# Kernel optimization log

Measured on AMD Instinct MI355X. Metric: run time of the kernel, lower is better.

## Reference

```python
import jax, jax.numpy as jnp
import numpy as np

D_MODEL = 768
NHEAD = 12
DK = D_MODEL // NHEAD
MAX_DIST = 1000.0
FF = 3072
POS_HIDDEN = 32  # hidden width of the relative-position bias MLP
EPS = 1e-5
B, L = 2, 1024


def setup_inputs() -> dict:
    key = jax.random.key(0)
    ks = jax.random.split(key, 24)

    def lin(k, i, o):  # torch-Linear-like init, stored as (in, out)
        return jax.random.uniform(k, (i, o), jnp.float32, -1.0, 1.0) / np.sqrt(i)

    return {
        "src": jax.random.normal(ks[0], (B, L, D_MODEL), jnp.float32),
        "src_x": jax.random.uniform(ks[1], (B, L), jnp.float32) * 1000.0,
        "src_y": jax.random.uniform(ks[2], (B, L), jnp.float32) * 1000.0,
        # attention projections (q,k,v,out)
        "Wq": lin(ks[3], D_MODEL, D_MODEL), "bq": jnp.zeros((D_MODEL,), jnp.float32),
        "Wk": lin(ks[4], D_MODEL, D_MODEL), "bk": jnp.zeros((D_MODEL,), jnp.float32),
        "Wv": lin(ks[5], D_MODEL, D_MODEL), "bv": jnp.zeros((D_MODEL,), jnp.float32),
        "Wo": lin(ks[6], D_MODEL, D_MODEL), "bo": jnp.zeros((D_MODEL,), jnp.float32),
        # relative-position bias MLP: 2 -> POS_HIDDEN -> NHEAD
        "P1": lin(ks[7], 2, POS_HIDDEN), "pb1": jnp.zeros((POS_HIDDEN,), jnp.float32),
        "P2": lin(ks[8], POS_HIDDEN, NHEAD), "pb2": jnp.zeros((NHEAD,), jnp.float32),
        # FFN
        "W1": lin(ks[9], D_MODEL, FF), "b1": jnp.zeros((FF,), jnp.float32),
        "W2": lin(ks[10], FF, D_MODEL), "b2": jnp.zeros((D_MODEL,), jnp.float32),
        # post-LN params
        "g1": jnp.ones((D_MODEL,), jnp.float32), "be1": jnp.zeros((D_MODEL,), jnp.float32),
        "g2": jnp.ones((D_MODEL,), jnp.float32), "be2": jnp.zeros((D_MODEL,), jnp.float32),
    }


def _layernorm(x, g, b):
    m = jnp.mean(x, axis=-1, keepdims=True)
    v = jnp.var(x, axis=-1, keepdims=True)
    return (x - m) * jax.lax.rsqrt(v + EPS) * g + b


def reference(src, src_x, src_y, Wq, bq, Wk, bk, Wv, bv, Wo, bo,
              P1, pb1, P2, pb2, W1, b1, W2, b2, g1, be1, g2, be2):
    b, l, _ = src.shape
    # projections -> (b, h, l, dk)
    q = (src @ Wq + bq).reshape(b, l, NHEAD, DK).transpose(0, 2, 1, 3)
    k = (src @ Wk + bk).reshape(b, l, NHEAD, DK).transpose(0, 2, 1, 3)
    v = (src @ Wv + bv).reshape(b, l, NHEAD, DK).transpose(0, 2, 1, 3)
    # 2D relative positions, clipped and normalized to [-1, 1]
    rx = jnp.clip(src_x[:, :, None] - src_x[:, None, :], -MAX_DIST, MAX_DIST) / MAX_DIST
    ry = jnp.clip(src_y[:, :, None] - src_y[:, None, :], -MAX_DIST, MAX_DIST) / MAX_DIST
    rel = jnp.stack([rx, ry], axis=-1)                        # (b, l, l, 2)
    bias = jax.nn.relu(rel @ P1 + pb1) @ P2 + pb2             # (b, l, l, h)
    bias = bias.transpose(0, 3, 1, 2)                         # (b, h, l, l)
    scores = jnp.einsum('bhqd,bhkd->bhqk', q, k) / np.sqrt(DK).astype(np.float32) + bias
    attn = jax.nn.softmax(scores, axis=-1)
    o = jnp.einsum('bhqk,bhkd->bhqd', attn, v).transpose(0, 2, 1, 3).reshape(b, l, D_MODEL)
    src2 = o @ Wo + bo
    x = _layernorm(src + src2, g1, be1)                       # post-LN residual 1
    ff = jax.nn.relu(x @ W1 + b1) @ W2 + b2                   # FFN
    return _layernorm(x + ff, g2, be2)                        # post-LN residual 2
```

## Files before the change

### kernel.cpp

```cpp
#include <hip/hip_runtime.h>
#include <math.h>

typedef unsigned short ushort_t;
typedef __attribute__((ext_vector_type(8))) short bf16x8;
typedef __attribute__((ext_vector_type(4))) float f32x4;

constexpr int kD      = 768;
constexpr int kNH     = 12;
constexpr int kDK     = 64;
constexpr int kFF     = 3072;
constexpr int kL      = 1024;
constexpr int kRows   = 2048;
constexpr float kEPS  = 1e-5f;

__device__ __forceinline__ ushort_t f2bf(float f) {
    union { float f; unsigned u; } v; v.f = f;
    unsigned r = (v.u + 0x7fffu + ((v.u >> 16) & 1u)) >> 16;
    return (ushort_t)r;
}
__device__ __forceinline__ float bf2f(ushort_t u) {
    union { unsigned u; float f; } v; v.u = ((unsigned)u) << 16; return v.f;
}

#define GL_LDS(gp, lp) __builtin_amdgcn_global_load_lds( \
    (const __attribute__((address_space(1))) void*)(gp), \
    (__attribute__((address_space(3))) void*)(lp), 16, 0, 0)

template<int RELU, int OUTBF, int ADDBIAS>
__device__ __forceinline__ void gemm_body(const ushort_t* __restrict__ A,
                                          const ushort_t* __restrict__ WT,
                                          const float* __restrict__ bias,
                                          void* __restrict__ Cout,
                                          int N, int K, int row0, int col0,
                                          int kbeg, int kend)
{
    __shared__ ushort_t lds[8192];
    ushort_t* As = lds;
    ushort_t* Bs = lds + 4096;

    const int tid  = threadIdx.x;
    const int lane = tid & 63;
    const int wave = tid >> 6;
    const int wrow = (wave & 1) * 64;
    const int wcol = (wave >> 1) * 64;

    const int srow = wave * 16 + (lane >> 2);
    const int sk   = (lane & 3) * 8;
    const ushort_t* ga0 = A  + (size_t)(row0 + srow)      * K + sk;
    const ushort_t* ga1 = A  + (size_t)(row0 + srow + 64) * K + sk;
    const ushort_t* gb0 = WT + (size_t)(col0 + srow)      * K + sk;
    const ushort_t* gb1 = WT + (size_t)(col0 + srow + 64) * K + sk;
    ushort_t* la0 = As + wave * 512;
    ushort_t* la1 = As + 2048 + wave * 512;
    ushort_t* lb0 = Bs + wave * 512;
    ushort_t* lb1 = Bs + 2048 + wave * 512;

    const int fl = lane & 15, fq = lane >> 4;
    const ushort_t* fa[4];
    const ushort_t* fb[4];
    #pragma unroll
    for (int i = 0; i < 4; ++i) {
        fa[i] = As + (wrow + i * 16 + fl) * 32 + fq * 8;
        fb[i] = Bs + (wcol + i * 16 + fl) * 32 + fq * 8;
    }

    f32x4 acc[4][4] = {};

    for (int k0 = kbeg; k0 < kend; k0 += 32) {
        __syncthreads();
        GL_LDS(ga0 + k0, la0);
        GL_LDS(ga1 + k0, la1);
        GL_LDS(gb0 + k0, lb0);
        GL_LDS(gb1 + k0, lb1);
        __syncthreads();

        bf16x8 av[4], bv[4];
        #pragma unroll
        for (int i = 0; i < 4; ++i) {
            av[i] = *(const bf16x8*)fa[i];
            bv[i] = *(const bf16x8*)fb[i];
        }
        #pragma unroll
        for (int mi = 0; mi < 4; ++mi)
            #pragma unroll
            for (int ni = 0; ni < 4; ++ni)
                acc[mi][ni] = __builtin_amdgcn_mfma_f32_16x16x32_bf16(
                    av[mi], bv[ni], acc[mi][ni], 0, 0, 0);
    }

    #pragma unroll
    for (int mi = 0; mi < 4; ++mi) {
        const int m = wrow + mi * 16 + fq * 4;
        #pragma unroll
        for (int ni = 0; ni < 4; ++ni) {
            const int n = wcol + ni * 16 + fl;
            const float bb = ADDBIAS ? bias[col0 + n] : 0.f;
            #pragma unroll
            for (int r = 0; r < 4; ++r) {
                float v = acc[mi][ni][r] + bb;
                if (RELU) v = fmaxf(v, 0.f);
                const size_t idx = (size_t)(row0 + m + r) * N + col0 + n;
                if (OUTBF) ((ushort_t*)Cout)[idx] = f2bf(v);
                else       ((float*)Cout)[idx]    = v;
            }
        }
    }
}

template<int RELU, int OUTBF>
__global__ __launch_bounds__(256)
void gemm_kernel(const ushort_t* __restrict__ A, const ushort_t* __restrict__ WT,
                 const float* __restrict__ bias, void* __restrict__ Cout,
                 int N, int K)
{
    gemm_body<RELU, OUTBF, 1>(A, WT, bias, Cout, N, K,
                              blockIdx.y * 128, blockIdx.x * 128, 0, K);
}

__global__ __launch_bounds__(256)
void gemm_splitk_kernel(const ushort_t* __restrict__ A, const ushort_t* __restrict__ WT,
                        float* __restrict__ parts, int N, int K, int kslice)
{
    const int z = blockIdx.z;
    float* out = parts + (size_t)z * kRows * N;
    gemm_body<0, 0, 0>(A, WT, nullptr, out, N, K,
                       blockIdx.y * 128, blockIdx.x * 128, z * kslice, (z + 1) * kslice);
}

__global__ __launch_bounds__(256)
void gemm_qkv_kernel(const ushort_t* __restrict__ A,
                     const ushort_t* wq, const ushort_t* wk, const ushort_t* wv,
                     const float* bq, const float* bk, const float* bv,
                     ushort_t* q, ushort_t* k, ushort_t* v)
{
    const ushort_t* WT; const float* bias; ushort_t* out;
    if (blockIdx.z == 0)      { WT = wq; bias = bq; out = q; }
    else if (blockIdx.z == 1) { WT = wk; bias = bk; out = k; }
    else                      { WT = wv; bias = bv; out = v; }
    gemm_body<0, 1, 1>(A, WT, bias, out, kD, kD,
                       blockIdx.y * 128, blockIdx.x * 128, 0, kD);
}

struct WtDesc { const float* src; ushort_t* dst; int K; int N; };
struct WtArgs { WtDesc d[3]; };

__global__ __launch_bounds__(256)
void wt_kernel(WtArgs args)
{
    const WtDesc w = args.d[blockIdx.z];
    const int ktiles = w.K >> 6;
    const int kt = (blockIdx.x % ktiles) * 64;
    const int nt = (blockIdx.x / ktiles) * 64;
    if (nt >= w.N) return;

    __shared__ float T[64][65];
    const int tid = threadIdx.x;
    #pragma unroll
    for (int i = 0; i < 4; ++i) {
        const int e = tid + i * 256;
        const int r = e >> 4;
        const int c = (e & 15) * 4;
        const float4 f = *(const float4*)&w.src[(size_t)(kt + r) * w.N + nt + c];
        T[c + 0][r] = f.x; T[c + 1][r] = f.y; T[c + 2][r] = f.z; T[c + 3][r] = f.w;
    }
    __syncthreads();
    #pragma unroll
    for (int i = 0; i < 4; ++i) {
        const int e = tid + i * 256;
        const int n = e >> 4;
        const int kc = (e & 15) * 4;
        ushort4 o;
        o.x = f2bf(T[n][kc + 0]); o.y = f2bf(T[n][kc + 1]);
        o.z = f2bf(T[n][kc + 2]); o.w = f2bf(T[n][kc + 3]);
        *(ushort4*)&w.dst[(size_t)(nt + n) * w.K + kt + kc] = o;
    }
}

__global__ __launch_bounds__(256)
void cvt_kernel(const float* __restrict__ in, ushort_t* __restrict__ out, int n4)
{
    const int i = blockIdx.x * 256 + threadIdx.x;
    if (i < n4) {
        const float4 f = ((const float4*)in)[i];
        ushort4 o;
        o.x = f2bf(f.x); o.y = f2bf(f.y); o.z = f2bf(f.z); o.w = f2bf(f.w);
        ((ushort4*)out)[i] = o;
    }
}

__global__ __launch_bounds__(256)
void vtrans_kernel(const ushort_t* __restrict__ vb, ushort_t* __restrict__ vt)
{
    const int bh = blockIdx.x;
    const int b = bh / kNH, h = bh - b * kNH;
    const int j0 = blockIdx.y * 64;
    __shared__ ushort_t T[64][72];

    const int tid = threadIdx.x;
    {
        const int jr = tid & 63;
        const int c0 = (tid >> 6) * 16;
        const ushort_t* sp = vb + (size_t)(b * kL + j0 + jr) * kD + h * kDK + c0;
        uint4 u0 = *(const uint4*)sp;
        uint4 u1 = *(const uint4*)(sp + 8);
        const ushort_t* e0 = (const ushort_t*)&u0;
        const ushort_t* e1 = (const ushort_t*)&u1;
        #pragma unroll
        for (int jj = 0; jj < 8; ++jj) {
            T[c0 + jj][jr]     = e0[jj];
            T[c0 + 8 + jj][jr] = e1[jj];
        }
    }
    __syncthreads();
    {
        const int dr = tid >> 2;
        const int jc = (tid & 3) * 16;
        ushort_t* dp = vt + (size_t)(bh * 64 + dr) * kL + j0 + jc;
        *(uint4*)dp       = *(const uint4*)&T[dr][jc];
        *(uint4*)(dp + 8) = *(const uint4*)&T[dr][jc + 8];
    }
}

__global__ __launch_bounds__(256)
void bias_kernel(const float* __restrict__ sx, const float* __restrict__ sy,
                 const float* __restrict__ P1, const float* __restrict__ pb1,
                 const float* __restrict__ P2, const float* __restrict__ pb2,
                 ushort_t* __restrict__ biasb)
{
    const int bid = blockIdx.x;
    const int b = bid >> 12;
    const int i = (bid >> 2) & 1023;
    const int j = (bid & 3) * 256 + threadIdx.x;
    const int tid = threadIdx.x;

    __shared__ float A1[32], B1[32], C1[32], W2l[384], pb2l[12];
    if (tid < 32) { A1[tid] = P1[tid]; B1[tid] = P1[32 + tid]; C1[tid] = pb1[tid]; }
    if (tid < 12) pb2l[tid] = pb2[tid];
    for (int e = tid; e < 384; e += 256) W2l[e] = P2[e];
    __syncthreads();

    const float xi = sx[b * kL + i], yi = sy[b * kL + i];
    float rx = xi - sx[b * kL + j];
    float ry = yi - sy[b * kL + j];
    rx = fminf(fmaxf(rx, -1000.f), 1000.f) * 1e-3f;
    ry = fminf(fmaxf(ry, -1000.f), 1000.f) * 1e-3f;

    float acc[12] = {};
    #pragma unroll
    for (int u = 0; u < 32; ++u) {
        float t = fmaf(rx, A1[u], fmaf(ry, B1[u], C1[u]));
        t = fmaxf(t, 0.f);
        #pragma unroll
        for (int h = 0; h < 12; ++h)
            acc[h] = fmaf(t, W2l[u * 12 + h], acc[h]);
    }
    #pragma unroll
    for (int h = 0; h < 12; ++h)
        biasb[((size_t)(b * kNH + h) * kL + i) * kL + j] = f2bf(acc[h] + pb2l[h]);
}

__global__ __launch_bounds__(64)
void attn_kernel(const ushort_t* __restrict__ qg, const ushort_t* __restrict__ kg,
                 const ushort_t* __restrict__ vt, const ushort_t* __restrict__ biasb,
                 ushort_t* __restrict__ og)
{
    const int bh = blockIdx.x;
    const int b  = bh / kNH, h = bh - b * kNH;
    const int q0 = blockIdx.y * 16;
    const int lane = threadIdx.x;
    const int fl = lane & 15, fq = lane >> 4;

    __shared__ ushort_t Sp[16][72];

    const size_t qoff = (size_t)(b * kL + q0 + fl) * kD + h * kDK + fq * 8;
    const bf16x8 aq0 = *(const bf16x8*)(qg + qoff);
    const bf16x8 aq1 = *(const bf16x8*)(qg + qoff + 32);

    const ushort_t* kbase = kg + (size_t)(b * kL) * kD + h * kDK;
    const ushort_t* vbase = vt + (size_t)(bh * 64) * kL;
    const ushort_t* bbase = biasb + ((size_t)bh * kL + q0) * kL;

    f32x4 accO[4] = {};
    float m_run[4] = {-INFINITY, -INFINITY, -INFINITY, -INFINITY};
    float l_run[4] = {};

    for (int k0 = 0; k0 < kL; k0 += 64) {
        float bvals[4][4];
        #pragma unroll
        for (int r = 0; r < 4; ++r)
            #pragma unroll
            for (int n = 0; n < 4; ++n)
                bvals[n][r] = bf2f(bbase[(size_t)(fq * 4 + r) * kL + k0 + n * 16 + fl]);

        f32x4 S[4] = {};
        #pragma unroll
        for (int n = 0; n < 4; ++n) {
            const ushort_t* kr = kbase + (size_t)(k0 + n * 16 + fl) * kD + fq * 8;
            const bf16x8 bk0 = *(const bf16x8*)kr;
            const bf16x8 bk1 = *(const bf16x8*)(kr + 32);
            S[n] = __builtin_amdgcn_mfma_f32_16x16x32_bf16(aq0, bk0, S[n], 0, 0, 0);
            S[n] = __builtin_amdgcn_mfma_f32_16x16x32_bf16(aq1, bk1, S[n], 0, 0, 0);
        }
        #pragma unroll
        for (int n = 0; n < 4; ++n)
            #pragma unroll
            for (int r = 0; r < 4; ++r)
                S[n][r] = fmaf(S[n][r], 0.125f, bvals[n][r]);

        #pragma unroll
        for (int r = 0; r < 4; ++r) {
            float mx = fmaxf(fmaxf(S[0][r], S[1][r]), fmaxf(S[2][r], S[3][r]));
            mx = fmaxf(mx, __shfl_xor(mx, 1, 16));
            mx = fmaxf(mx, __shfl_xor(mx, 2, 16));
            mx = fmaxf(mx, __shfl_xor(mx, 4, 16));
            mx = fmaxf(mx, __shfl_xor(mx, 8, 16));
            const float mnew  = fmaxf(m_run[r], mx);
            const float alpha = __expf(m_run[r] - mnew);
            float ls = 0.f;
            #pragma unroll
            for (int n = 0; n < 4; ++n) {
                const float e = __expf(S[n][r] - mnew);
                S[n][r] = e;
                ls += e;
            }
            ls += __shfl_xor(ls, 1, 16);
            ls += __shfl_xor(ls, 2, 16);
            ls += __shfl_xor(ls, 4, 16);
            ls += __shfl_xor(ls, 8, 16);
            l_run[r] = l_run[r] * alpha + ls;
            m_run[r] = mnew;
            #pragma unroll
            for (int n = 0; n < 4; ++n) accO[n][r] *= alpha;
        }

        #pragma unroll
        for (int n = 0; n < 4; ++n)
            #pragma unroll
            for (int r = 0; r < 4; ++r)
                Sp[fq * 4 + r][n * 16 + fl] = f2bf(S[n][r]);
        __syncthreads();

        const bf16x8 ap0 = *(const bf16x8*)&Sp[fl][fq * 8];
        const bf16x8 ap1 = *(const bf16x8*)&Sp[fl][32 + fq * 8];
        #pragma unroll
        for (int n = 0; n < 4; ++n) {
            const ushort_t* vr = vbase + (size_t)(n * 16 + fl) * kL + k0 + fq * 8;
            const bf16x8 bv0 = *(const bf16x8*)vr;
            const bf16x8 bv1 = *(const bf16x8*)(vr + 32);
            accO[n] = __builtin_amdgcn_mfma_f32_16x16x32_bf16(ap0, bv0, accO[n], 0, 0, 0);
            accO[n] = __builtin_amdgcn_mfma_f32_16x16x32_bf16(ap1, bv1, accO[n], 0, 0, 0);
        }
        __syncthreads();
    }

    float inv[4];
    #pragma unroll
    for (int r = 0; r < 4; ++r) inv[r] = 1.0f / l_run[r];
    #pragma unroll
    for (int n = 0; n < 4; ++n)
        #pragma unroll
        for (int r = 0; r < 4; ++r)
            og[(size_t)(b * kL + q0 + fq * 4 + r) * kD + h * kDK + n * 16 + fl] =
                f2bf(accO[n][r] * inv[r]);
}

template<int NPART, int DUAL>
__global__ __launch_bounds__(256)
void ln_kernel(const float* __restrict__ a, const float* __restrict__ parts,
               const float* __restrict__ bias,
               const float* __restrict__ g, const float* __restrict__ be,
               float* __restrict__ out, ushort_t* __restrict__ out_bf)
{
    const int row = blockIdx.x;
    const int tid = threadIdx.x;
    const float* pa = a + (size_t)row * kD;
    constexpr size_t NTOK = (size_t)kRows * kD;

    float v[3];
    float s = 0.f, sq = 0.f;
    #pragma unroll
    for (int i = 0; i < 3; ++i) {
        const int d = tid + i * 256;
        float t = pa[d] + bias[d];
        #pragma unroll
        for (int p = 0; p < NPART; ++p)
            t += parts[p * NTOK + (size_t)row * kD + d];
        v[i] = t;
        s  += t;
        sq += t * t;
    }
    #pragma unroll
    for (int off = 32; off > 0; off >>= 1) {
        s  += __shfl_down(s, off);
        sq += __shfl_down(sq, off);
    }
    __shared__ float bs[4], bq2[4];
    if ((tid & 63) == 0) { bs[tid >> 6] = s; bq2[tid >> 6] = sq; }
    __syncthreads();
    const float ts = bs[0] + bs[1] + bs[2] + bs[3];
    const float tq = bq2[0] + bq2[1] + bq2[2] + bq2[3];
    const float invn = 1.0f / (float)kD;
    const float mean = ts * invn;
    const float var  = tq * invn - mean * mean;
    const float rstd = rsqrtf(var + kEPS);

    float* po = out + (size_t)row * kD;
    #pragma unroll
    for (int i = 0; i < 3; ++i) {
        const int d = tid + i * 256;
        const float o = (v[i] - mean) * rstd * g[d] + be[d];
        po[d] = o;
        if (DUAL) out_bf[(size_t)row * kD + d] = f2bf(o);
    }
}

extern "C" void kernel_launch(void* const* d_in, const int* in_sizes, int n_in,
                              void* d_out, int out_size, void* d_ws, size_t ws_size,
                              hipStream_t stream)
{
    const float* src = (const float*)d_in[0];
    const float* sx  = (const float*)d_in[1];
    const float* sy  = (const float*)d_in[2];
    const float* Wq  = (const float*)d_in[3];  const float* bq  = (const float*)d_in[4];
    const float* Wk  = (const float*)d_in[5];  const float* bk  = (const float*)d_in[6];
    const float* Wv  = (const float*)d_in[7];  const float* bv  = (const float*)d_in[8];
    const float* Wo  = (const float*)d_in[9];  const float* bo  = (const float*)d_in[10];
    const float* P1  = (const float*)d_in[11]; const float* pb1 = (const float*)d_in[12];
    const float* P2  = (const float*)d_in[13]; const float* pb2 = (const float*)d_in[14];
    const float* W1  = (const float*)d_in[15]; const float* b1  = (const float*)d_in[16];
    const float* W2  = (const float*)d_in[17]; const float* b2  = (const float*)d_in[18];
    const float* g1  = (const float*)d_in[19]; const float* be1 = (const float*)d_in[20];
    const float* g2  = (const float*)d_in[21]; const float* be2 = (const float*)d_in[22];

    constexpr size_t W768  = 768u * 768u;
    constexpr size_t W3072 = 768u * 3072u;
    constexpr size_t NTOK  = (size_t)kRows * kD;

    ushort_t* wsu = (ushort_t*)d_ws;
    ushort_t* wqT = wsu;
    ushort_t* wkT = wqT + W768;
    ushort_t* wvT = wkT + W768;
    ushort_t* qb  = wvT + W768;
    ushort_t* kb  = qb + NTOK;
    ushort_t* vb  = kb + NTOK;
    ushort_t* sb  = vb + NTOK;
    ushort_t* vtb = sb + NTOK;
    ushort_t* biasb = vtb + NTOK;
    ushort_t* woT   = biasb;
    ushort_t* w1T   = woT + W768;
    ushort_t* w2T   = w1T + W3072;
    float*    xb    = (float*)(w2T + W3072);
    ushort_t* h1bf  = (ushort_t*)(xb + NTOK);
    float*    s2p   = (float*)h1bf;
    float*    ff2p  = (float*)(h1bf + 4 * NTOK);
    ushort_t* xbf   = qb;

    const dim3 blk(256);

    WtArgs wa_early;
    wa_early.d[0] = { Wq, wqT, kD, kD };
    wa_early.d[1] = { Wk, wkT, kD, kD };
    wa_early.d[2] = { Wv, wvT, kD, kD };
    wt_kernel<<<dim3(144, 1, 3), blk, 0, stream>>>(wa_early);
    cvt_kernel<<<dim3((int)(NTOK / 4 / 256)), blk, 0, stream>>>(src, sb, (int)(NTOK / 4));
    bias_kernel<<<dim3(8192), blk, 0, stream>>>(sx, sy, P1, pb1, P2, pb2, biasb);

    gemm_qkv_kernel<<<dim3(kD / 128, kRows / 128, 3), blk, 0, stream>>>(
        sb, wqT, wkT, wvT, bq, bk, bv, qb, kb, vb);

    vtrans_kernel<<<dim3(2 * kNH, kL / 64), blk, 0, stream>>>(vb, vtb);

    attn_kernel<<<dim3(2 * kNH, kL / 16), dim3(64), 0, stream>>>(qb, kb, vtb, biasb, sb);

    WtArgs wa_late;
    wa_late.d[0] = { Wo, woT, kD,  kD  };
    wa_late.d[1] = { W1, w1T, kD,  kFF };
    wa_late.d[2] = { W2, w2T, kFF, kD  };
    wt_kernel<<<dim3(576, 1, 3), blk, 0, stream>>>(wa_late);

    gemm_splitk_kernel<<<dim3(kD / 128, kRows / 128, 2), blk, 0, stream>>>(
        sb, woT, s2p, kD, kD, kD / 2);

    ln_kernel<2, 1><<<dim3(kRows), blk, 0, stream>>>(src, s2p, bo, g1, be1, xb, xbf);

    gemm_kernel<1, 1><<<dim3(kFF / 128, kRows / 128), blk, 0, stream>>>(
        xbf, w1T, b1, h1bf, kFF, kD);

    gemm_splitk_kernel<<<dim3(kD / 128, kRows / 128, 3), blk, 0, stream>>>(
        h1bf, w2T, ff2p, kD, kFF, kFF / 3);

    ln_kernel<3, 0><<<dim3(kRows), blk, 0, stream>>>(xb, ff2p, b2, g2, be2,
                                                     (float*)d_out, nullptr);
}
```

Baseline: 310.3 us.

## Split attention over key halves, pre-tile bias, prefetch K and bias

```diff
diff --git a/kernel.cpp b/kernel.cpp
--- a/kernel.cpp
+++ b/kernel.cpp
@@ -12,6 +12,7 @@
 constexpr int kL      = 1024;
 constexpr int kRows   = 2048;
 constexpr float kEPS  = 1e-5f;
+constexpr int kMLRows = 24 * kL;
 
 __device__ __forceinline__ ushort_t f2bf(float f) {
     union { float f; unsigned u; } v; v.f = f;
@@ -228,45 +229,75 @@
                  ushort_t* __restrict__ biasb)
 {
     const int bid = blockIdx.x;
-    const int b = bid >> 12;
-    const int i = (bid >> 2) & 1023;
-    const int j = (bid & 3) * 256 + threadIdx.x;
+    const int b  = bid >> 10;
+    const int qt = (bid >> 4) & 63;
+    const int kt = bid & 15;
     const int tid = threadIdx.x;
 
     __shared__ float A1[32], B1[32], C1[32], W2l[384], pb2l[12];
+    __shared__ float qxl[16], qyl[16], kxl[64], kyl[64];
+    __shared__ ushort_t Btile[12 * 1024];
+
     if (tid < 32) { A1[tid] = P1[tid]; B1[tid] = P1[32 + tid]; C1[tid] = pb1[tid]; }
     if (tid < 12) pb2l[tid] = pb2[tid];
     for (int e = tid; e < 384; e += 256) W2l[e] = P2[e];
+    if (tid < 16) { qxl[tid] = sx[b * kL + qt * 16 + tid];
+                    qyl[tid] = sy[b * kL + qt * 16 + tid]; }
+    if (tid < 64) { kxl[tid] = sx[b * kL + kt * 64 + tid];
+                    kyl[tid] = sy[b * kL + kt * 64 + tid]; }
     __syncthreads();
 
-    const float xi = sx[b * kL + i], yi = sy[b * kL + i];
-    float rx = xi - sx[b * kL + j];
-    float ry = yi - sy[b * kL + j];
-    rx = fminf(fmaxf(rx, -1000.f), 1000.f) * 1e-3f;
-    ry = fminf(fmaxf(ry, -1000.f), 1000.f) * 1e-3f;
-
-    float acc[12] = {};
-    #pragma unroll
-    for (int u = 0; u < 32; ++u) {
-        float t = fmaf(rx, A1[u], fmaf(ry, B1[u], C1[u]));
-        t = fmaxf(t, 0.f);
+    const int ri = tid >> 4;
+    const int fl = tid & 15;
+    const int fq = ri >> 2, r = ri & 3;
+    const int lane = fq * 16 + fl;
+    const float xi = qxl[ri], yi = qyl[ri];
+
+    #pragma unroll
+    for (int nn = 0; nn < 4; ++nn) {
+        const int n  = nn ^ (fl >> 2);
+        const int cj = n * 16 + fl;
+        float rx = xi - kxl[cj];
+        float ry = yi - kyl[cj];
+        rx = fminf(fmaxf(rx, -1000.f), 1000.f) * 1e-3f;
+        ry = fminf(fmaxf(ry, -1000.f), 1000.f) * 1e-3f;
+
+        float acc[12] = {};
+        #pragma unroll
+        for (int u = 0; u < 32; ++u) {
+            float t = fmaf(rx, A1[u], fmaf(ry, B1[u], C1[u]));
+            t = fmaxf(t, 0.f);
+            #pragma unroll
+            for (int h = 0; h < 12; ++h)
+                acc[h] = fmaf(t, W2l[u * 12 + h], acc[h]);
+        }
         #pragma unroll
         for (int h = 0; h < 12; ++h)
-            acc[h] = fmaf(t, W2l[u * 12 + h], acc[h]);
-    }
-    #pragma unroll
-    for (int h = 0; h < 12; ++h)
-        biasb[((size_t)(b * kNH + h) * kL + i) * kL + j] = f2bf(acc[h] + pb2l[h]);
-}
-
-__global__ __launch_bounds__(64)
+            Btile[h * 1024 + lane * 16 + n * 4 + r] = f2bf(acc[h] + pb2l[h]);
+    }
+    __syncthreads();
+
+    #pragma unroll
+    for (int pass = 0; pass < 6; ++pass) {
+        const int h = pass * 2 + (tid >> 7);
+        const int inner = (tid & 127) * 8;
+        ushort_t* dst = biasb +
+            (((size_t)(b * kNH + h) * 64 + qt) * 16 + kt) * 1024 + inner;
+        *(uint4*)dst = *(const uint4*)&Btile[h * 1024 + inner];
+    }
+}
+
+__global__ __launch_bounds__(64, 3)
 void attn_kernel(const ushort_t* __restrict__ qg, const ushort_t* __restrict__ kg,
                  const ushort_t* __restrict__ vt, const ushort_t* __restrict__ biasb,
-                 ushort_t* __restrict__ og)
+                 ushort_t* __restrict__ p0, ushort_t* __restrict__ p1,
+                 float2* __restrict__ ml)
 {
     const int bh = blockIdx.x;
     const int b  = bh / kNH, h = bh - b * kNH;
-    const int q0 = blockIdx.y * 16;
+    const int qt = blockIdx.y;
+    const int q0 = qt * 16;
+    const int z  = blockIdx.z;
     const int lane = threadIdx.x;
     const int fl = lane & 15, fq = lane >> 4;
 
@@ -276,36 +307,69 @@
     const bf16x8 aq0 = *(const bf16x8*)(qg + qoff);
     const bf16x8 aq1 = *(const bf16x8*)(qg + qoff + 32);
 
-    const ushort_t* kbase = kg + (size_t)(b * kL) * kD + h * kDK;
-    const ushort_t* vbase = vt + (size_t)(bh * 64) * kL;
-    const ushort_t* bbase = biasb + ((size_t)bh * kL + q0) * kL;
+    const ushort_t* kbase = kg + (size_t)(b * kL) * kD + h * kDK + fq * 8;
+    const ushort_t* vbase = vt + (size_t)(bh * 64) * kL + fq * 8;
+    const ushort_t* btile = biasb +
+        ((size_t)(bh * 64 + qt) * 16 + z * 8) * 1024 + lane * 16;
 
     f32x4 accO[4] = {};
     float m_run[4] = {-INFINITY, -INFINITY, -INFINITY, -INFINITY};
     float l_run[4] = {};
 
-    for (int k0 = 0; k0 < kL; k0 += 64) {
-        float bvals[4][4];
-        #pragma unroll
-        for (int r = 0; r < 4; ++r)
-            #pragma unroll
-            for (int n = 0; n < 4; ++n)
-                bvals[n][r] = bf2f(bbase[(size_t)(fq * 4 + r) * kL + k0 + n * 16 + fl]);
+    bf16x8 kc[4][2];
+    uint4 bc0, bc1;
+    {
+        const int k0 = z * 512;
+        #pragma unroll
+        for (int n = 0; n < 4; ++n) {
+            const ushort_t* kr = kbase + (size_t)(k0 + n * 16 + fl) * kD;
+            kc[n][0] = *(const bf16x8*)kr;
+            kc[n][1] = *(const bf16x8*)(kr + 32);
+        }
+        bc0 = *(const uint4*)btile;
+        bc1 = *(const uint4*)(btile + 8);
+    }
+
+    #pragma unroll
+    for (int t = 0; t < 8; ++t) {
+        const int k0 = z * 512 + t * 64;
+
+        bf16x8 vv[4][2];
+        #pragma unroll
+        for (int n = 0; n < 4; ++n) {
+            const ushort_t* vr = vbase + (size_t)(n * 16 + fl) * kL + k0;
+            vv[n][0] = *(const bf16x8*)vr;
+            vv[n][1] = *(const bf16x8*)(vr + 32);
+        }
 
         f32x4 S[4] = {};
         #pragma unroll
         for (int n = 0; n < 4; ++n) {
-            const ushort_t* kr = kbase + (size_t)(k0 + n * 16 + fl) * kD + fq * 8;
-            const bf16x8 bk0 = *(const bf16x8*)kr;
-            const bf16x8 bk1 = *(const bf16x8*)(kr + 32);
-            S[n] = __builtin_amdgcn_mfma_f32_16x16x32_bf16(aq0, bk0, S[n], 0, 0, 0);
-            S[n] = __builtin_amdgcn_mfma_f32_16x16x32_bf16(aq1, bk1, S[n], 0, 0, 0);
-        }
+            S[n] = __builtin_amdgcn_mfma_f32_16x16x32_bf16(aq0, kc[n][0], S[n], 0, 0, 0);
+            S[n] = __builtin_amdgcn_mfma_f32_16x16x32_bf16(aq1, kc[n][1], S[n], 0, 0, 0);
+        }
+
+        bf16x8 kn[4][2];
+        uint4 bn0, bn1;
+        if (t < 7) {
+            #pragma unroll
+            for (int n = 0; n < 4; ++n) {
+                const ushort_t* kr = kbase + (size_t)(k0 + 64 + n * 16 + fl) * kD;
+                kn[n][0] = *(const bf16x8*)kr;
+                kn[n][1] = *(const bf16x8*)(kr + 32);
+            }
+            bn0 = *(const uint4*)(btile + (t + 1) * 1024);
+            bn1 = *(const uint4*)(btile + (t + 1) * 1024 + 8);
+        }
+
+        ushort_t bu[16];
+        *(uint4*)&bu[0] = bc0;
+        *(uint4*)&bu[8] = bc1;
         #pragma unroll
         for (int n = 0; n < 4; ++n)
             #pragma unroll
             for (int r = 0; r < 4; ++r)
-                S[n][r] = fmaf(S[n][r], 0.125f, bvals[n][r]);
+                S[n][r] = fmaf(S[n][r], 0.125f, bf2f(bu[n * 4 + r]));
 
         #pragma unroll
         for (int r = 0; r < 4; ++r) {
@@ -344,15 +408,19 @@
         const bf16x8 ap1 = *(const bf16x8*)&Sp[fl][32 + fq * 8];
         #pragma unroll
         for (int n = 0; n < 4; ++n) {
-            const ushort_t* vr = vbase + (size_t)(n * 16 + fl) * kL + k0 + fq * 8;
-            const bf16x8 bv0 = *(const bf16x8*)vr;
-            const bf16x8 bv1 = *(const bf16x8*)(vr + 32);
-            accO[n] = __builtin_amdgcn_mfma_f32_16x16x32_bf16(ap0, bv0, accO[n], 0, 0, 0);
-            accO[n] = __builtin_amdgcn_mfma_f32_16x16x32_bf16(ap1, bv1, accO[n], 0, 0, 0);
+            accO[n] = __builtin_amdgcn_mfma_f32_16x16x32_bf16(ap0, vv[n][0], accO[n], 0, 0, 0);
+            accO[n] = __builtin_amdgcn_mfma_f32_16x16x32_bf16(ap1, vv[n][1], accO[n], 0, 0, 0);
         }
         __syncthreads();
-    }
-
+
+        if (t < 7) {
+            #pragma unroll
+            for (int n = 0; n < 4; ++n) { kc[n][0] = kn[n][0]; kc[n][1] = kn[n][1]; }
+            bc0 = bn0; bc1 = bn1;
+        }
+    }
+
+    ushort_t* p = z ? p1 : p0;
     float inv[4];
     #pragma unroll
     for (int r = 0; r < 4; ++r) inv[r] = 1.0f / l_run[r];
@@ -360,8 +428,43 @@
     for (int n = 0; n < 4; ++n)
         #pragma unroll
         for (int r = 0; r < 4; ++r)
-            og[(size_t)(b * kL + q0 + fq * 4 + r) * kD + h * kDK + n * 16 + fl] =
+            p[(size_t)(b * kL + q0 + fq * 4 + r) * kD + h * kDK + n * 16 + fl] =
                 f2bf(accO[n][r] * inv[r]);
+    if (fl == 0) {
+        #pragma unroll
+        for (int r = 0; r < 4; ++r)
+            ml[(size_t)z * kMLRows + bh * kL + q0 + fq * 4 + r] =
+                make_float2(m_run[r], l_run[r]);
+    }
+}
+
+__global__ __launch_bounds__(256)
+void attn_combine_kernel(const ushort_t* __restrict__ p0, const ushort_t* __restrict__ p1,
+                         const float2* __restrict__ ml, ushort_t* __restrict__ out)
+{
+    const int tid = threadIdx.x;
+    const int R = blockIdx.x * 32 + (tid >> 3);
+    const int bh = R >> 10, i = R & 1023;
+    const int b = bh / kNH, h = bh - b * kNH;
+
+    const float2 s0 = ml[bh * kL + i];
+    const float2 s1 = ml[kMLRows + bh * kL + i];
+    const float M  = fmaxf(s0.x, s1.x);
+    const float w0 = __expf(s0.x - M) * s0.y;
+    const float w1 = __expf(s1.x - M) * s1.y;
+    const float inv = 1.0f / (w0 + w1);
+    const float c0 = w0 * inv, c1 = w1 * inv;
+
+    const size_t base = (size_t)(b * kL + i) * kD + h * kDK + (tid & 7) * 8;
+    uint4 u0 = *(const uint4*)(p0 + base);
+    uint4 u1 = *(const uint4*)(p1 + base);
+    const ushort_t* e0 = (const ushort_t*)&u0;
+    const ushort_t* e1 = (const ushort_t*)&u1;
+    ushort_t o[8];
+    #pragma unroll
+    for (int j = 0; j < 8; ++j)
+        o[j] = f2bf(c0 * bf2f(e0[j]) + c1 * bf2f(e1[j]));
+    *(uint4*)(out + base) = *(const uint4*)o;
 }
 
 template<int NPART, int DUAL>
@@ -453,6 +556,7 @@
     ushort_t* h1bf  = (ushort_t*)(xb + NTOK);
     float*    s2p   = (float*)h1bf;
     float*    ff2p  = (float*)(h1bf + 4 * NTOK);
+    float2*   mlb   = (float2*)wqT;
     ushort_t* xbf   = qb;
 
     const dim3 blk(256);
@@ -463,14 +567,16 @@
     wa_early.d[2] = { Wv, wvT, kD, kD };
     wt_kernel<<<dim3(144, 1, 3), blk, 0, stream>>>(wa_early);
     cvt_kernel<<<dim3((int)(NTOK / 4 / 256)), blk, 0, stream>>>(src, sb, (int)(NTOK / 4));
-    bias_kernel<<<dim3(8192), blk, 0, stream>>>(sx, sy, P1, pb1, P2, pb2, biasb);
+    bias_kernel<<<dim3(2048), blk, 0, stream>>>(sx, sy, P1, pb1, P2, pb2, biasb);
 
     gemm_qkv_kernel<<<dim3(kD / 128, kRows / 128, 3), blk, 0, stream>>>(
         sb, wqT, wkT, wvT, bq, bk, bv, qb, kb, vb);
 
     vtrans_kernel<<<dim3(2 * kNH, kL / 64), blk, 0, stream>>>(vb, vtb);
 
-    attn_kernel<<<dim3(2 * kNH, kL / 16), dim3(64), 0, stream>>>(qb, kb, vtb, biasb, sb);
+    attn_kernel<<<dim3(2 * kNH, kL / 16, 2), dim3(64), 0, stream>>>(
+        qb, kb, vtb, biasb, sb, vb, mlb);
+    attn_combine_kernel<<<dim3(768), blk, 0, stream>>>(sb, vb, mlb, qb);
 
     WtArgs wa_late;
     wa_late.d[0] = { Wo, woT, kD,  kD  };
@@ -479,7 +585,7 @@
     wt_kernel<<<dim3(576, 1, 3), blk, 0, stream>>>(wa_late);
 
     gemm_splitk_kernel<<<dim3(kD / 128, kRows / 128, 2), blk, 0, stream>>>(
-        sb, woT, s2p, kD, kD, kD / 2);
+        qb, woT, s2p, kD, kD, kD / 2);
 
     ln_kernel<2, 1><<<dim3(kRows), blk, 0, stream>>>(src, s2p, bo, g1, be1, xb, xbf);
 
```

After: 428.8 us. +38.2%, slower.
